# Kernel tuning notes

Hardware: AMD Instinct MI355X
Metric: run time of the kernel (lower is better)

## Reference

```python
import jax, jax.numpy as jnp
import numpy as np
import math

C, H, L, V = 1024, 16, 2, 32000
D = C // H  # head_dim = 64
FF = 4 * C
B, T = 1, 2048
EPS = 1e-5

def _alibi_slopes(n_heads):
    start = 2 ** (-2 ** (-(math.log2(n_heads) - 3)))
    return np.array([start * start ** i for i in range(n_heads)], dtype=np.float32)

SLOPES = jnp.asarray(_alibi_slopes(H))

def _sym_ln(x, w, b):
    # per-head-channel LayerNorm over head_dim, scalar scale/bias per head
    xh = x.reshape(x.shape[0], x.shape[1], H, D)
    mu = xh.mean(-1, keepdims=True)
    var = ((xh - mu) ** 2).mean(-1, keepdims=True)
    n = (xh - mu) / jnp.sqrt(var + EPS)
    n = n * w[None, None, :, None] + b[None, None, :, None]
    return n.reshape(x.shape)

def _alibi_bias(t):
    pos = jnp.arange(t)[None, :] - jnp.arange(t)[:, None]  # j - i
    pos = jnp.minimum(pos, 0).astype(jnp.float32)
    return SLOPES[:, None, None] * pos[None, :, :]  # (H, T, T)

def _block(x, ln1_w, ln1_b, ln2_w, ln2_b, attn_w, attn_b, v_tmp, proj_tmp, fc_w, fc_b, pw, pb):
    b_, t_, _ = x.shape
    h_in = _sym_ln(x, ln1_w, ln1_b)
    qk = h_in @ attn_w.T + attn_b  # (B, T, 2C)
    q, k = jnp.split(qk, 2, axis=-1)
    # Kronecker/block-diagonal V: per-head (head_dim x head_dim) matmul, x @ M^T per head
    xh = h_in.reshape(b_, t_, H, D)
    v = jnp.einsum('bthd,hed->bthe', xh, v_tmp)  # (B, T, H, D)
    q = q.reshape(b_, t_, H, D).transpose(0, 2, 1, 3)
    k = k.reshape(b_, t_, H, D).transpose(0, 2, 1, 3)
    v = v.transpose(0, 2, 1, 3)
    scale = 1.0 / math.sqrt(D)
    scores = jnp.einsum('bhqd,bhkd->bhqk', q, k) * scale
    scores = scores + _alibi_bias(t_)[None]  # note: no causal mask in original code
    att = jax.nn.softmax(scores, axis=-1)
    y = jnp.einsum('bhqk,bhkd->bhqd', att, v)
    y = y.transpose(0, 2, 1, 3)  # (B, T, H, D)
    y = jnp.einsum('bthd,hed->bthe', y, proj_tmp).reshape(b_, t_, C)
    x = x + y
    h2 = _sym_ln(x, ln2_w, ln2_b)
    f = jax.nn.gelu(h2 @ fc_w.T + fc_b, approximate=False)
    x = x + (f @ pw.T + pb)
    return x

def setup_inputs() -> dict:
    key = jax.random.key(0)
    ks = jax.random.split(key, 12)
    s = 0.02
    return {
        'idx': jax.random.randint(ks[0], (B, T), 0, V, dtype=jnp.int32),
        'wte': jax.random.normal(ks[1], (V, C), jnp.float32) * s,
        'ln1_w': jnp.ones((L, H), jnp.float32),
        'ln1_b': jnp.zeros((L, H), jnp.float32),
        'ln2_w': jnp.ones((L, H), jnp.float32),
        'ln2_b': jnp.zeros((L, H), jnp.float32),
        'lnf_w': jnp.ones((H,), jnp.float32),
        'lnf_b': jnp.zeros((H,), jnp.float32),
        'attn_w': jax.random.normal(ks[2], (L, 2 * C, C), jnp.float32) * s,
        'attn_b': jnp.zeros((L, 2 * C), jnp.float32),
        'v_tmp': jax.random.normal(ks[3], (L, H, D, D), jnp.float32) * s,
        'proj_tmp': jax.random.normal(ks[4], (L, H, D, D), jnp.float32) * s,
        'fc_w': jax.random.normal(ks[5], (L, FF, C), jnp.float32) * s,
        'fc_b': jnp.zeros((L, FF), jnp.float32),
        'proj_w': jax.random.normal(ks[6], (L, C, FF), jnp.float32) * s,
        'proj_b': jnp.zeros((L, C), jnp.float32),
    }

def reference(idx, wte, ln1_w, ln1_b, ln2_w, ln2_b, lnf_w, lnf_b,
              attn_w, attn_b, v_tmp, proj_tmp, fc_w, fc_b, proj_w, proj_b):
    x = wte[idx]  # (B, T, C)
    for l in range(L):
        x = _block(x, ln1_w[l], ln1_b[l], ln2_w[l], ln2_b[l],
                   attn_w[l], attn_b[l], v_tmp[l], proj_tmp[l],
                   fc_w[l], fc_b[l], proj_w[l], proj_b[l])
    x = _sym_ln(x, lnf_w, lnf_b)
    logits = x @ wte.T  # tied lm_head
    return logits
```

## Files before the change

### kernel.cpp

```cpp
#include <hip/hip_runtime.h>
#include <cstdint>
#include <cstddef>

#define T_SEQ 2048
#define C_DIM 1024
#define H_HEADS 16
#define D_HEAD 64
#define FF_DIM 4096
#define V_VOCAB 32000
#define L_LAYERS 2

typedef unsigned short u16;
typedef short bf16x8 __attribute__((ext_vector_type(8)));
typedef float f32x4 __attribute__((ext_vector_type(4)));

__device__ inline u16 f2bf(float f) {
  unsigned u = __float_as_uint(f);
  u += 0x7fffu + ((u >> 16) & 1u);
  return (u16)(u >> 16);
}
__device__ inline float bf2f(u16 h) { return __uint_as_float(((unsigned)h) << 16); }

#define OFF_WTEBF   0ULL
#define OFF_ATTNBF  65536000ULL
#define OFF_FCBF    73924608ULL
#define OFF_PRJBF   90701824ULL
#define OFF_X       107479040ULL
#define OFF_HBF     115867648ULL
#define OFF_QKBF    120061952ULL
#define OFF_VT      128450560ULL
#define OFF_FBF     141033472ULL
#define OFF_VWBF    157810688ULL
#define OFF_PWBF    158072832ULL
#define ARENA_BYTES 158334976ULL

__device__ __align__(1024) unsigned char g_arena[ARENA_BYTES];

__global__ void cvt_embed_k(const float4* __restrict__ sw, const float4* __restrict__ s0,
                            const float4* __restrict__ s1, const float4* __restrict__ s2,
                            const float4* __restrict__ s3, const float4* __restrict__ s4,
                            ushort4* __restrict__ dw, ushort4* __restrict__ d0,
                            ushort4* __restrict__ d1, ushort4* __restrict__ d2,
                            ushort4* __restrict__ d3, ushort4* __restrict__ d4,
                            const int* __restrict__ idx, float4* __restrict__ x,
                            const float* __restrict__ lw, const float* __restrict__ lb,
                            ushort4* __restrict__ hout) {
  int blk = blockIdx.x, tid = threadIdx.x;
  if (blk < 52736) {
    int g = blk * 256 + tid;
    const float4* s; ushort4* d; int off;
    if (g < 8192000)       { s = sw; d = dw; off = g; }
    else {
      int g2 = g - 8192000;
      if (g2 < 1048576)      { s = s0; d = d0; off = g2; }
      else if (g2 < 3145728) { s = s1; d = d1; off = g2 - 1048576; }
      else if (g2 < 5242880) { s = s2; d = d2; off = g2 - 3145728; }
      else if (g2 < 5275648) { s = s3; d = d3; off = g2 - 5242880; }
      else                   { s = s4; d = d4; off = g2 - 5275648; }
    }
    float4 v = s[off];
    d[off] = make_ushort4(f2bf(v.x), f2bf(v.y), f2bf(v.z), f2bf(v.w));
  } else {
    int t = blk - 52736;
    int r = idx[t];
    float4 v = sw[(size_t)r * 256 + tid];
    x[(size_t)t * 256 + tid] = v;
    float s = v.x + v.y + v.z + v.w;
    float s2 = v.x * v.x + v.y * v.y + v.z * v.z + v.w * v.w;
    #pragma unroll
    for (int m = 1; m <= 8; m <<= 1) { s += __shfl_xor(s, m); s2 += __shfl_xor(s2, m); }
    int h = tid >> 4;
    float mu = s * (1.f / 64.f), var = s2 * (1.f / 64.f) - mu * mu;
    float rs = rsqrtf(var + 1e-5f) * lw[h], b = lb[h];
    hout[(size_t)t * 256 + tid] =
        make_ushort4(f2bf((v.x - mu) * rs + b), f2bf((v.y - mu) * rs + b),
                     f2bf((v.z - mu) * rs + b), f2bf((v.w - mu) * rs + b));
  }
}

template <int NROWS, int ROWBYTES, int WAVES>
__device__ inline void stage_rows(u16* lds, const u16* __restrict__ g, int ld,
                                  int wid, int lane) {
  constexpr int PASSES = (NROWS * ROWBYTES) / (WAVES * 1024);
  #pragma unroll
  for (int i = 0; i < PASSES; i++) {
    int base = (i * WAVES + wid) * 1024;
    int o = base + lane * 16;
    int u = o ^ (((o / ROWBYTES) & 7) << 4);
    int row = u / ROWBYTES, colb = u % ROWBYTES;
    const u16* src = g + (size_t)row * ld + (colb >> 1);
    __builtin_amdgcn_global_load_lds((const __attribute__((address_space(1))) void*)src,
                                     (__attribute__((address_space(3))) void*)(lds + base / 2),
                                     16, 0, 0);
  }
}

__device__ inline void stage_pass(u16* lds, const u16* __restrict__ g, int ld,
                                  int i, int wid, int lane) {
  int base = (i * 8 + wid) * 1024;
  int o = base + lane * 16;
  int u = o ^ (((o >> 7) & 7) << 4);
  int row = u >> 7, colb = u & 127;
  const u16* src = g + (size_t)row * ld + (colb >> 1);
  __builtin_amdgcn_global_load_lds((const __attribute__((address_space(1))) void*)src,
                                   (__attribute__((address_space(3))) void*)(lds + base / 2),
                                   16, 0, 0);
}

__global__ __launch_bounds__(256) void flash_k(const u16* __restrict__ qk,
                                               const u16* __restrict__ vt,
                                               const u16* __restrict__ pw,
                                               float* __restrict__ x,
                                               const float* __restrict__ ln2w,
                                               const float* __restrict__ ln2b,
                                               u16* __restrict__ hout) {
  int h = blockIdx.y;
  int q0 = blockIdx.x * 64;
  int tid = threadIdx.x, wid = tid >> 6, lane = tid & 63;
  int g4 = lane >> 4, l15 = lane & 15;
  __shared__ u16 Kl[128 * 64];
  __shared__ u16 Vl[64 * 128];
  __shared__ u16 Pl[64 * 128];
  float slopeL = exp2f(-0.5f * (float)(h + 1)) * 1.44269504f;

  bf16x8 qf[2];
  const u16* qb = qk + (size_t)(q0 + wid * 16) * 2048 + h * 64;
  #pragma unroll
  for (int kk = 0; kk < 2; kk++)
    qf[kk] = *(const bf16x8*)(qb + (size_t)l15 * 2048 + kk * 32 + g4 * 8);

  float lsum = 0.f;
  f32x4 oacc[4];
  #pragma unroll
  for (int n = 0; n < 4; n++) oacc[n] = (f32x4){0.f, 0.f, 0.f, 0.f};

  const u16* kbase = qk + 1024 + h * 64;
  const u16* vbase = vt + (size_t)h * 64 * T_SEQ;
  int myq = q0 + wid * 16 + l15;

  for (int kt = 0; kt < T_SEQ / 128; kt++) {
    int k0 = kt * 128;
    stage_rows<128, 128, 4>(Kl, kbase + (size_t)k0 * 2048, 2048, wid, lane);
    stage_rows<64, 256, 4>(Vl, vbase + k0, T_SEQ, wid, lane);
    __syncthreads();

    f32x4 s[8];
    #pragma unroll
    for (int n = 0; n < 8; n++) s[n] = (f32x4){0.f, 0.f, 0.f, 0.f};
    #pragma unroll
    for (int kk = 0; kk < 2; kk++) {
      #pragma unroll
      for (int n = 0; n < 8; n++) {
        int r = n * 16 + l15;
        int b = (r * 128 + kk * 64 + g4 * 16) ^ ((r & 7) << 4);
        bf16x8 kf = *(const bf16x8*)((const char*)Kl + b);
        s[n] = __builtin_amdgcn_mfma_f32_16x16x32_bf16(kf, qf[kk], s[n], 0, 0, 0);
      }
    }

    float fd = (float)(k0 + g4 * 4 - myq);
    int pr = wid * 16 + l15;
    #pragma unroll
    for (int n = 0; n < 8; n++) {
      float p[4];
      #pragma unroll
      for (int i = 0; i < 4; i++) {
        float dj = fd + (float)(n * 16 + i);
        float a2 = fmaf(slopeL, fminf(dj, 0.f), -11.54156036f);
        p[i] = exp2f(fmaf(s[n][i], 0.18033688f, a2));
        lsum += p[i];
      }
      unsigned lo, hi;
      asm("v_cvt_pk_bf16_f32 %0, %1, %2" : "=v"(lo) : "v"(p[0]), "v"(p[1]));
      asm("v_cvt_pk_bf16_f32 %0, %1, %2" : "=v"(hi) : "v"(p[2]), "v"(p[3]));
      int b = (pr * 256 + n * 32 + g4 * 8) ^ ((pr & 7) << 4);
      *(uint2*)((char*)Pl + b) = make_uint2(lo, hi);
    }

    #pragma unroll
    for (int kk = 0; kk < 4; kk++) {
      int pb = (pr * 256 + kk * 64 + g4 * 16) ^ ((pr & 7) << 4);
      bf16x8 pa = *(const bf16x8*)((const char*)Pl + pb);
      #pragma unroll
      for (int n = 0; n < 4; n++) {
        int d = n * 16 + l15;
        int vb = (d * 256 + kk * 64 + g4 * 16) ^ ((d & 7) << 4);
        bf16x8 vf = *(const bf16x8*)((const char*)Vl + vb);
        oacc[n] = __builtin_amdgcn_mfma_f32_16x16x32_bf16(pa, vf, oacc[n], 0, 0, 0);
      }
    }
    __syncthreads();
  }

  lsum += __shfl_xor(lsum, 16);
  lsum += __shfl_xor(lsum, 32);
  float linv[4];
  #pragma unroll
  for (int i = 0; i < 4; i++) linv[i] = 1.f / __shfl(lsum, g4 * 4 + i);

  stage_rows<64, 128, 4>(Kl, pw + (size_t)h * 4096, 64, wid, lane);
  #pragma unroll
  for (int n = 0; n < 4; n++)
    #pragma unroll
    for (int i = 0; i < 4; i++) {
      int pr = wid * 16 + g4 * 4 + i;
      int b = (pr * 256 + (n * 16 + l15) * 2) ^ ((pr & 7) << 4);
      *(u16*)((char*)Pl + b) = f2bf(oacc[n][i] * linv[i]);
    }
  __syncthreads();

  f32x4 acc2[4];
  #pragma unroll
  for (int n = 0; n < 4; n++) acc2[n] = (f32x4){0.f, 0.f, 0.f, 0.f};
  #pragma unroll
  for (int kk = 0; kk < 2; kk++) {
    int pr = wid * 16 + l15;
    int ab = (pr * 256 + kk * 64 + g4 * 16) ^ ((pr & 7) << 4);
    bf16x8 af = *(const bf16x8*)((const char*)Pl + ab);
    #pragma unroll
    for (int n = 0; n < 4; n++) {
      int r = n * 16 + l15;
      int wb = (r * 128 + kk * 64 + g4 * 16) ^ ((r & 7) << 4);
      bf16x8 wf = *(const bf16x8*)((const char*)Kl + wb);
      acc2[n] = __builtin_amdgcn_mfma_f32_16x16x32_bf16(af, wf, acc2[n], 0, 0, 0);
    }
  }

  float* xb = x + (size_t)(q0 + wid * 16) * C_DIM + h * 64;
  u16* hb = hout + (size_t)(q0 + wid * 16) * C_DIM + h * 64;
  float xv[4][4];
  #pragma unroll
  for (int n = 0; n < 4; n++)
    #pragma unroll
    for (int i = 0; i < 4; i++) {
      size_t o = (size_t)(g4 * 4 + i) * C_DIM + n * 16 + l15;
      float t = xb[o] + acc2[n][i];
      xb[o] = t;
      xv[n][i] = t;
    }
  float lw = ln2w[h], lb = ln2b[h];
  #pragma unroll
  for (int i = 0; i < 4; i++) {
    float s = 0.f, s2 = 0.f;
    #pragma unroll
    for (int n = 0; n < 4; n++) { float t = xv[n][i]; s += t; s2 += t * t; }
    #pragma unroll
    for (int m = 1; m <= 8; m <<= 1) { s += __shfl_xor(s, m); s2 += __shfl_xor(s2, m); }
    float mu = s * (1.f / 64.f), var = s2 * (1.f / 64.f) - mu * mu;
    float rs = rsqrtf(var + 1e-5f) * lw;
    #pragma unroll
    for (int n = 0; n < 4; n++)
      hb[(size_t)(g4 * 4 + i) * C_DIM + n * 16 + l15] = f2bf((xv[n][i] - mu) * rs + lb);
  }
}

#define ASM_VMCNT0 asm volatile("s_waitcnt vmcnt(0)" ::: "memory")

__global__ __launch_bounds__(512, 1) void gemm256_k(const u16* __restrict__ A, int lda,
                                                    const u16* __restrict__ B, int ldb,
                                                    float* __restrict__ C, int ldc,
                                                    int K, int MT) {
  extern __shared__ u16 sm[];
  u16* lsA = sm;
  u16* lsB = sm + 32768;
  int tid = threadIdx.x, wid = tid >> 6, lane = tid & 63;
  int g4 = lane >> 4, l15 = lane & 15;
  int wm = wid >> 2, wn = wid & 3;
  int nwg = gridDim.x, lin = blockIdx.x;
  int chunk = nwg >> 3;
  int w = (lin & 7) * chunk + (lin >> 3);
  int by = w % MT, bx = w / MT;
  const u16* Ab = A + (size_t)(by * 256) * lda;
  const u16* Bb = B + (size_t)(bx * 256) * ldb;

  f32x4 acc[8][4];
  #pragma unroll
  for (int m = 0; m < 8; m++)
    #pragma unroll
    for (int n = 0; n < 4; n++) acc[m][n] = (f32x4){0.f, 0.f, 0.f, 0.f};

  int NT = K >> 6;
  stage_rows<256, 128, 8>(lsA, Ab, lda, wid, lane);
  stage_rows<256, 128, 8>(lsB, Bb, ldb, wid, lane);

  for (int t = 0; t < NT; ++t) {
    int cur = t & 1;
    const char* cA = (const char*)(lsA + cur * 16384);
    const char* cB = (const char*)(lsB + cur * 16384);
    u16* nAl = lsA + (cur ^ 1) * 16384;
    u16* nBl = lsB + (cur ^ 1) * 16384;
    const u16* gA = Ab + (t + 1) * 64;
    const u16* gB = Bb + (t + 1) * 64;
    bool pf = (t + 1 < NT);

    ASM_VMCNT0;
    __builtin_amdgcn_s_barrier();
    __builtin_amdgcn_sched_barrier(0);

    bf16x8 bfr[4], af[4];
    #pragma unroll
    for (int ph = 0; ph < 4; ++ph) {
      const int kk = ph >> 1, mh = ph & 1;
      if (mh == 0) {
        #pragma unroll
        for (int n = 0; n < 4; n++) {
          int r = wn * 64 + n * 16 + l15;
          bfr[n] = *(const bf16x8*)(cB + ((r * 128 + kk * 64 + g4 * 16) ^ ((r & 7) << 4)));
        }
      }
      #pragma unroll
      for (int m = 0; m < 4; m++) {
        int r = wm * 128 + mh * 64 + m * 16 + l15;
        af[m] = *(const bf16x8*)(cA + ((r * 128 + kk * 64 + g4 * 16) ^ ((r & 7) << 4)));
      }
      if (pf) {
        if (ph == 0) { stage_pass(nAl, gA, lda, 0, wid, lane);
                       stage_pass(nAl, gA, lda, 1, wid, lane);
                       stage_pass(nBl, gB, ldb, 0, wid, lane); }
        else if (ph == 1) { stage_pass(nAl, gA, lda, 2, wid, lane);
                            stage_pass(nAl, gA, lda, 3, wid, lane);
                            stage_pass(nBl, gB, ldb, 1, wid, lane); }
        else if (ph == 2) { stage_pass(nBl, gB, ldb, 2, wid, lane);
                            stage_pass(nBl, gB, ldb, 3, wid, lane); }
      }
      __builtin_amdgcn_s_setprio(1);
      #pragma unroll
      for (int m = 0; m < 4; m++)
        #pragma unroll
        for (int n = 0; n < 4; n++)
          acc[mh * 4 + m][n] =
              __builtin_amdgcn_mfma_f32_16x16x32_bf16(af[m], bfr[n], acc[mh * 4 + m][n], 0, 0, 0);
      __builtin_amdgcn_s_setprio(0);
      __builtin_amdgcn_s_barrier();
    }
  }

  int gr0 = by * 256 + wm * 128, gc0 = bx * 256 + wn * 64;
  #pragma unroll
  for (int m = 0; m < 8; m++)
    #pragma unroll
    for (int n = 0; n < 4; n++)
      #pragma unroll
      for (int i = 0; i < 4; i++)
        C[(size_t)(gr0 + m * 16 + g4 * 4 + i) * ldc + gc0 + n * 16 + l15] = acc[m][n][i];
}

template <int BM, int BN, int WM, int WN, int EPI, int MT, int GRID>
__global__ void gemm_nt(const u16* __restrict__ A, int lda, long long sA,
                        const u16* __restrict__ B, int ldb, long long sB,
                        void* __restrict__ C, int ldc, long long sC,
                        int K, const float* __restrict__ bias,
                        const float* __restrict__ resid, int ldr,
                        const float* __restrict__ lnw, const float* __restrict__ lnb,
                        u16* __restrict__ hout) {
  constexpr int RM = BM / WM, RN = BN / WN;
  constexpr int MR = RM / 16, NR = RN / 16;
  __shared__ u16 lsA[BM * 64];
  __shared__ u16 lsB[BN * 64];
  int tid = threadIdx.x, wid = tid >> 6, lane = tid & 63;
  int wm = wid / WN, wn = wid % WN;
  int lin, z;
  if constexpr (GRID == 1) {
    lin = blockIdx.x; z = blockIdx.y;
  } else {
    int nwg = gridDim.x, l0 = blockIdx.x;
    int chunk = nwg >> 3;
    lin = (l0 & 7) * chunk + (l0 >> 3);
    z = 0;
  }
  int by = lin % MT, bx = lin / MT;
  int row0 = by * BM, col0 = bx * BN;
  const u16* Ab = A + (size_t)z * sA + (size_t)row0 * lda;
  const u16* Bb = B + (size_t)z * sB + (size_t)col0 * ldb;
  size_t cz = (size_t)z * sC;

  f32x4 acc[MR][NR];
  #pragma unroll
  for (int m = 0; m < MR; m++)
    #pragma unroll
    for (int n = 0; n < NR; n++) acc[m][n] = (f32x4){0.f, 0.f, 0.f, 0.f};

  for (int k0 = 0; k0 < K; k0 += 64) {
    stage_rows<BM, 128, 4>(lsA, Ab + k0, lda, wid, lane);
    stage_rows<BN, 128, 4>(lsB, Bb + k0, ldb, wid, lane);
    __syncthreads();
    #pragma unroll
    for (int kk = 0; kk < 2; kk++) {
      bf16x8 af[MR], bfr[NR];
      #pragma unroll
      for (int m = 0; m < MR; m++) {
        int r = wm * RM + m * 16 + (lane & 15);
        int bofs = (r * 128 + kk * 64 + ((lane >> 4) * 16)) ^ ((r & 7) << 4);
        af[m] = *(const bf16x8*)((const char*)lsA + bofs);
      }
      #pragma unroll
      for (int n = 0; n < NR; n++) {
        int r = wn * RN + n * 16 + (lane & 15);
        int bofs = (r * 128 + kk * 64 + ((lane >> 4) * 16)) ^ ((r & 7) << 4);
        bfr[n] = *(const bf16x8*)((const char*)lsB + bofs);
      }
      #pragma unroll
      for (int m = 0; m < MR; m++)
        #pragma unroll
        for (int n = 0; n < NR; n++)
          acc[m][n] = __builtin_amdgcn_mfma_f32_16x16x32_bf16(af[m], bfr[n], acc[m][n], 0, 0, 0);
    }
    __syncthreads();
  }

  int rbase = row0 + wm * RM, cbase = col0 + wn * RN;
  if constexpr (EPI == 6) {
    float vv[MR][NR][4];
    #pragma unroll
    for (int m = 0; m < MR; m++)
      #pragma unroll
      for (int n = 0; n < NR; n++)
        #pragma unroll
        for (int i = 0; i < 4; i++) {
          int gr = rbase + m * 16 + ((lane >> 4) * 4) + i;
          int gc = cbase + n * 16 + (lane & 15);
          float v = acc[m][n][i] + bias[gc] + resid[(size_t)gr * ldr + gc];
          vv[m][n][i] = v;
          ((float*)C)[(size_t)gr * ldc + gc] = v;
        }
    int h = cbase >> 6;
    float lw = lnw[h], lb = lnb[h];
    #pragma unroll
    for (int m = 0; m < MR; m++)
      #pragma unroll
      for (int i = 0; i < 4; i++) {
        float s = 0.f, s2 = 0.f;
        #pragma unroll
        for (int n = 0; n < NR; n++) { float t = vv[m][n][i]; s += t; s2 += t * t; }
        #pragma unroll
        for (int msk = 1; msk <= 8; msk <<= 1) { s += __shfl_xor(s, msk); s2 += __shfl_xor(s2, msk); }
        float mu = s * (1.f / 64.f), var = s2 * (1.f / 64.f) - mu * mu;
        float rs = rsqrtf(var + 1e-5f) * lw;
        int gr = rbase + m * 16 + ((lane >> 4) * 4) + i;
        #pragma unroll
        for (int n = 0; n < NR; n++) {
          int gc = cbase + n * 16 + (lane & 15);
          hout[(size_t)gr * C_DIM + gc] = f2bf((vv[m][n][i] - mu) * rs + lb);
        }
      }
  } else {
    #pragma unroll
    for (int m = 0; m < MR; m++)
      #pragma unroll
      for (int n = 0; n < NR; n++)
        #pragma unroll
        for (int i = 0; i < 4; i++) {
          int gr = rbase + m * 16 + ((lane >> 4) * 4) + i;
          int gc = cbase + n * 16 + (lane & 15);
          size_t idx = cz + (size_t)gr * ldc + gc;
          float v = acc[m][n][i];
          if constexpr (EPI == 1) {
            v += bias[gc];
            ((u16*)C)[idx] = f2bf(v);
          } else if constexpr (EPI == 2) {
            ((u16*)C)[idx] = f2bf(v);
          } else if constexpr (EPI == 3) {
            v += bias[gc];
            v = 0.5f * v * (1.f + erff(v * 0.70710678118654752f));
            ((u16*)C)[idx] = f2bf(v);
          }
        }
  }
}

extern "C" void kernel_launch(void* const* d_in, const int* in_sizes, int n_in,
                              void* d_out, int out_size, void* d_ws, size_t ws_size,
                              hipStream_t stream) {
  (void)in_sizes; (void)n_in; (void)out_size; (void)d_ws; (void)ws_size;
  const int*   idx    = (const int*)d_in[0];
  const float* wte    = (const float*)d_in[1];
  const float* ln1w   = (const float*)d_in[2];
  const float* ln1b   = (const float*)d_in[3];
  const float* ln2w   = (const float*)d_in[4];
  const float* ln2b   = (const float*)d_in[5];
  const float* lnfw   = (const float*)d_in[6];
  const float* lnfb   = (const float*)d_in[7];
  const float* attw   = (const float*)d_in[8];
  const float* attb   = (const float*)d_in[9];
  const float* vtmp   = (const float*)d_in[10];
  const float* ptmp   = (const float*)d_in[11];
  const float* fcw    = (const float*)d_in[12];
  const float* fcb    = (const float*)d_in[13];
  const float* prjw   = (const float*)d_in[14];
  const float* prjb   = (const float*)d_in[15];
  float* out = (float*)d_out;

  unsigned char* ar = nullptr;
  (void)hipGetSymbolAddress((void**)&ar, HIP_SYMBOL(g_arena));
  u16*   wtebf  = (u16*)(ar + OFF_WTEBF);
  u16*   attnbf = (u16*)(ar + OFF_ATTNBF);
  u16*   fcbf   = (u16*)(ar + OFF_FCBF);
  u16*   prjbf  = (u16*)(ar + OFF_PRJBF);
  float* x      = (float*)(ar + OFF_X);
  u16*   hbf    = (u16*)(ar + OFF_HBF);
  u16*   qkbf   = (u16*)(ar + OFF_QKBF);
  u16*   vt     = (u16*)(ar + OFF_VT);
  u16*   fbf    = (u16*)(ar + OFF_FBF);
  u16*   vwbf   = (u16*)(ar + OFF_VWBF);
  u16*   pwbf   = (u16*)(ar + OFF_PWBF);

  (void)hipFuncSetAttribute((const void*)gemm256_k,
                            hipFuncAttributeMaxDynamicSharedMemorySize, 131072);

  cvt_embed_k<<<dim3(52736 + T_SEQ), 256, 0, stream>>>(
      (const float4*)wte, (const float4*)attw, (const float4*)fcw,
      (const float4*)prjw, (const float4*)vtmp, (const float4*)ptmp,
      (ushort4*)wtebf, (ushort4*)attnbf, (ushort4*)fcbf,
      (ushort4*)prjbf, (ushort4*)vwbf, (ushort4*)pwbf,
      idx, (float4*)x, ln1w, ln1b, (ushort4*)hbf);

  for (int l = 0; l < L_LAYERS; l++) {
    gemm_nt<64, 128, 2, 2, 1, 32, 0><<<dim3((2 * C_DIM / 128) * (T_SEQ / 64)), 256, 0, stream>>>(
        hbf, C_DIM, 0, attnbf + (size_t)l * 2 * C_DIM * C_DIM, C_DIM, 0,
        qkbf, 2 * C_DIM, 0, C_DIM, attb + l * 2 * C_DIM, nullptr, 0,
        nullptr, nullptr, nullptr);
    gemm_nt<64, 128, 2, 2, 2, 1, 1><<<dim3(T_SEQ / 128, H_HEADS), 256, 0, stream>>>(
        vwbf + (size_t)l * H_HEADS * 4096, 64, 4096, hbf, C_DIM, 64,
        vt, T_SEQ, (long long)64 * T_SEQ, 64, nullptr, nullptr, 0,
        nullptr, nullptr, nullptr);
    flash_k<<<dim3(T_SEQ / 64, H_HEADS), 256, 0, stream>>>(
        qkbf, vt, pwbf + (size_t)l * H_HEADS * 4096, x,
        ln2w + l * H_HEADS, ln2b + l * H_HEADS, hbf);
    gemm_nt<64, 128, 2, 2, 3, 32, 0><<<dim3((FF_DIM / 128) * (T_SEQ / 64)), 256, 0, stream>>>(
        hbf, C_DIM, 0, fcbf + (size_t)l * FF_DIM * C_DIM, C_DIM, 0,
        fbf, FF_DIM, 0, C_DIM, fcb + l * FF_DIM, nullptr, 0,
        nullptr, nullptr, nullptr);
    const float* nw = (l + 1 < L_LAYERS) ? ln1w + (l + 1) * H_HEADS : lnfw;
    const float* nb = (l + 1 < L_LAYERS) ? ln1b + (l + 1) * H_HEADS : lnfb;
    gemm_nt<32, 128, 2, 2, 6, 64, 0><<<dim3((C_DIM / 128) * (T_SEQ / 32)), 256, 0, stream>>>(
        fbf, FF_DIM, 0, prjbf + (size_t)l * C_DIM * FF_DIM, FF_DIM, 0,
        x, C_DIM, 0, FF_DIM, prjb + l * C_DIM, x, C_DIM,
        nw, nb, hbf);
  }
  gemm256_k<<<dim3((V_VOCAB / 256) * (T_SEQ / 256)), 512, 131072, stream>>>(
      hbf, C_DIM, wtebf, C_DIM, out, V_VOCAB, C_DIM, T_SEQ / 256);
}
```

Measured before the change: 507.6 us.

## Merge QK and V projection launches into one kernel; raise MFMA priority in attention

The QK projection GEMM and the per-head V projection GEMM are combined into a single qkv_k launch. Block IDs below 512 run the QK tile and the remaining 256 run the V tiles, using a shared device-side gemm_body. This removes one kernel launch per layer and lets the small V GEMM fill idle CUs alongside the QK tiles. The flash attention kernel also wraps its two MFMA phases in s_setprio(1)/s_setprio(0) to favour matrix issue over the softmax/exp work of other waves. The merged kernel still allocates LDS at the QK tile size, which could affect occupancy.

```diff
diff --git a/kernel.cpp b/kernel.cpp
--- a/kernel.cpp
+++ b/kernel.cpp
@@ -147,6 +147,7 @@
     f32x4 s[8];
     #pragma unroll
     for (int n = 0; n < 8; n++) s[n] = (f32x4){0.f, 0.f, 0.f, 0.f};
+    __builtin_amdgcn_s_setprio(1);
     #pragma unroll
     for (int kk = 0; kk < 2; kk++) {
       #pragma unroll
@@ -157,6 +158,7 @@
         s[n] = __builtin_amdgcn_mfma_f32_16x16x32_bf16(kf, qf[kk], s[n], 0, 0, 0);
       }
     }
+    __builtin_amdgcn_s_setprio(0);
 
     float fd = (float)(k0 + g4 * 4 - myq);
     int pr = wid * 16 + l15;
@@ -177,6 +179,7 @@
       *(uint2*)((char*)Pl + b) = make_uint2(lo, hi);
     }
 
+    __builtin_amdgcn_s_setprio(1);
     #pragma unroll
     for (int kk = 0; kk < 4; kk++) {
       int pb = (pr * 256 + kk * 64 + g4 * 16) ^ ((pr & 7) << 4);
@@ -189,6 +192,7 @@
         oacc[n] = __builtin_amdgcn_mfma_f32_16x16x32_bf16(pa, vf, oacc[n], 0, 0, 0);
       }
     }
+    __builtin_amdgcn_s_setprio(0);
     __syncthreads();
   }
 
@@ -345,29 +349,19 @@
         C[(size_t)(gr0 + m * 16 + g4 * 4 + i) * ldc + gc0 + n * 16 + l15] = acc[m][n][i];
 }
 
-template <int BM, int BN, int WM, int WN, int EPI, int MT, int GRID>
-__global__ void gemm_nt(const u16* __restrict__ A, int lda, long long sA,
-                        const u16* __restrict__ B, int ldb, long long sB,
-                        void* __restrict__ C, int ldc, long long sC,
-                        int K, const float* __restrict__ bias,
-                        const float* __restrict__ resid, int ldr,
-                        const float* __restrict__ lnw, const float* __restrict__ lnb,
-                        u16* __restrict__ hout) {
+template <int BM, int BN, int WM, int WN, int EPI, int MT>
+__device__ void gemm_body(u16* lsA, u16* lsB,
+                          const u16* __restrict__ A, int lda, long long sA,
+                          const u16* __restrict__ B, int ldb, long long sB,
+                          void* __restrict__ C, int ldc, long long sC,
+                          int K, const float* __restrict__ bias,
+                          const float* __restrict__ resid, int ldr,
+                          const float* __restrict__ lnw, const float* __restrict__ lnb,
+                          u16* __restrict__ hout, int lin, int z) {
   constexpr int RM = BM / WM, RN = BN / WN;
   constexpr int MR = RM / 16, NR = RN / 16;
-  __shared__ u16 lsA[BM * 64];
-  __shared__ u16 lsB[BN * 64];
   int tid = threadIdx.x, wid = tid >> 6, lane = tid & 63;
   int wm = wid / WN, wn = wid % WN;
-  int lin, z;
-  if constexpr (GRID == 1) {
-    lin = blockIdx.x; z = blockIdx.y;
-  } else {
-    int nwg = gridDim.x, l0 = blockIdx.x;
-    int chunk = nwg >> 3;
-    lin = (l0 & 7) * chunk + (l0 >> 3);
-    z = 0;
-  }
   int by = lin % MT, bx = lin / MT;
   int row0 = by * BM, col0 = bx * BN;
   const u16* Ab = A + (size_t)z * sA + (size_t)row0 * lda;
@@ -465,6 +459,43 @@
             ((u16*)C)[idx] = f2bf(v);
           }
         }
+  }
+}
+
+template <int BM, int BN, int WM, int WN, int EPI, int MT>
+__global__ void gemm_nt(const u16* __restrict__ A, int lda,
+                        const u16* __restrict__ B, int ldb,
+                        void* __restrict__ C, int ldc,
+                        int K, const float* __restrict__ bias,
+                        const float* __restrict__ resid, int ldr,
+                        const float* __restrict__ lnw, const float* __restrict__ lnb,
+                        u16* __restrict__ hout) {
+  __shared__ u16 lsA[BM * 64];
+  __shared__ u16 lsB[BN * 64];
+  int nwg = gridDim.x, l0 = blockIdx.x;
+  int chunk = nwg >> 3;
+  int lin = (l0 & 7) * chunk + (l0 >> 3);
+  gemm_body<BM, BN, WM, WN, EPI, MT>(lsA, lsB, A, lda, 0, B, ldb, 0, C, ldc, 0,
+                                     K, bias, resid, ldr, lnw, lnb, hout, lin, 0);
+}
+
+__global__ void qkv_k(const u16* __restrict__ hbf, const u16* __restrict__ attw,
+                      const float* __restrict__ attb, u16* __restrict__ qkbf,
+                      const u16* __restrict__ vw, u16* __restrict__ vt) {
+  __shared__ u16 lsA[64 * 64];
+  __shared__ u16 lsB[128 * 64];
+  int l0 = blockIdx.x;
+  if (l0 < 512) {
+    int lin = (l0 & 7) * 64 + (l0 >> 3);
+    gemm_body<64, 128, 2, 2, 1, 32>(lsA, lsB, hbf, C_DIM, 0, attw, C_DIM, 0,
+                                    qkbf, 2 * C_DIM, 0, C_DIM, attb, nullptr, 0,
+                                    nullptr, nullptr, nullptr, lin, 0);
+  } else {
+    int i2 = l0 - 512;
+    gemm_body<64, 128, 2, 2, 2, 1>(lsA, lsB, vw, 64, 4096, hbf, C_DIM, 64,
+                                   vt, T_SEQ, (long long)64 * T_SEQ, 64,
+                                   nullptr, nullptr, 0, nullptr, nullptr, nullptr,
+                                   i2 & 15, i2 >> 4);
   }
 }
 
@@ -515,26 +546,21 @@
       idx, (float4*)x, ln1w, ln1b, (ushort4*)hbf);
 
   for (int l = 0; l < L_LAYERS; l++) {
-    gemm_nt<64, 128, 2, 2, 1, 32, 0><<<dim3((2 * C_DIM / 128) * (T_SEQ / 64)), 256, 0, stream>>>(
-        hbf, C_DIM, 0, attnbf + (size_t)l * 2 * C_DIM * C_DIM, C_DIM, 0,
-        qkbf, 2 * C_DIM, 0, C_DIM, attb + l * 2 * C_DIM, nullptr, 0,
-        nullptr, nullptr, nullptr);
-    gemm_nt<64, 128, 2, 2, 2, 1, 1><<<dim3(T_SEQ / 128, H_HEADS), 256, 0, stream>>>(
-        vwbf + (size_t)l * H_HEADS * 4096, 64, 4096, hbf, C_DIM, 64,
-        vt, T_SEQ, (long long)64 * T_SEQ, 64, nullptr, nullptr, 0,
-        nullptr, nullptr, nullptr);
+    qkv_k<<<dim3(768), 256, 0, stream>>>(
+        hbf, attnbf + (size_t)l * 2 * C_DIM * C_DIM, attb + l * 2 * C_DIM, qkbf,
+        vwbf + (size_t)l * H_HEADS * 4096, vt);
     flash_k<<<dim3(T_SEQ / 64, H_HEADS), 256, 0, stream>>>(
         qkbf, vt, pwbf + (size_t)l * H_HEADS * 4096, x,
         ln2w + l * H_HEADS, ln2b + l * H_HEADS, hbf);
-    gemm_nt<64, 128, 2, 2, 3, 32, 0><<<dim3((FF_DIM / 128) * (T_SEQ / 64)), 256, 0, stream>>>(
-        hbf, C_DIM, 0, fcbf + (size_t)l * FF_DIM * C_DIM, C_DIM, 0,
-        fbf, FF_DIM, 0, C_DIM, fcb + l * FF_DIM, nullptr, 0,
+    gemm_nt<64, 128, 2, 2, 3, 32><<<dim3((FF_DIM / 128) * (T_SEQ / 64)), 256, 0, stream>>>(
+        hbf, C_DIM, fcbf + (size_t)l * FF_DIM * C_DIM, C_DIM,
+        fbf, FF_DIM, C_DIM, fcb + l * FF_DIM, nullptr, 0,
         nullptr, nullptr, nullptr);
     const float* nw = (l + 1 < L_LAYERS) ? ln1w + (l + 1) * H_HEADS : lnfw;
     const float* nb = (l + 1 < L_LAYERS) ? ln1b + (l + 1) * H_HEADS : lnfb;
-    gemm_nt<32, 128, 2, 2, 6, 64, 0><<<dim3((C_DIM / 128) * (T_SEQ / 32)), 256, 0, stream>>>(
-        fbf, FF_DIM, 0, prjbf + (size_t)l * C_DIM * FF_DIM, FF_DIM, 0,
-        x, C_DIM, 0, FF_DIM, prjb + l * C_DIM, x, C_DIM,
+    gemm_nt<32, 128, 2, 2, 6, 64><<<dim3((C_DIM / 128) * (T_SEQ / 32)), 256, 0, stream>>>(
+        fbf, FF_DIM, prjbf + (size_t)l * C_DIM * FF_DIM, FF_DIM,
+        x, C_DIM, FF_DIM, prjb + l * C_DIM, x, C_DIM,
         nw, nb, hbf);
   }
   gemm256_k<<<dim3((V_VOCAB / 256) * (T_SEQ / 256)), 512, 131072, stream>>>(
```

Measured after the change: 499.4 us, median of 2. No clear change (-1.6%).
